# Kernel optimization log

Measured on AMD Instinct MI355X. Metric: run time of the kernel, lower is better.

Reference implementation:

```python
import jax, jax.numpy as jnp
import numpy as np

N, E, F_IN, H, C = 50000, 800000, 64, 4, 32
NEG_SLOPE = 0.2  # PyG GATConv default negative_slope
LN_EPS = 1e-5


def setup_inputs() -> dict:
    key = jax.random.key(0)
    ks = jax.random.split(key, 8)
    s = 1.0 / np.sqrt(F_IN)
    return {
        "x": jax.random.normal(ks[0], (N, F_IN), jnp.float32),
        "edge_index": jax.random.randint(ks[1], (2, E), 0, N, jnp.int64),
        "W": jax.random.normal(ks[2], (F_IN, H * C), jnp.float32) * s,
        "att_src": jax.random.normal(ks[3], (H, C), jnp.float32) * s,
        "att_dst": jax.random.normal(ks[4], (H, C), jnp.float32) * s,
        "bias": jnp.zeros((H * C,), jnp.float32),
        "res_w": jax.random.normal(ks[5], (F_IN, H * C), jnp.float32) * s,
        "res_b": jnp.zeros((H * C,), jnp.float32),
        "ln_g": jnp.ones((H * C,), jnp.float32),
        "ln_b": jnp.zeros((H * C,), jnp.float32),
    }


def reference(x, edge_index, W, att_src, att_dst, bias, res_w, res_b, ln_g, ln_b):
    n = x.shape[0]
    # GATConv adds self-loops by default
    loop = jnp.arange(n, dtype=edge_index.dtype)
    src = jnp.concatenate([edge_index[0], loop])
    dst = jnp.concatenate([edge_index[1], loop])

    h = (x @ W).reshape(n, H, C)                      # [N,H,C]
    a_src = jnp.einsum('nhc,hc->nh', h, att_src)       # [N,H]
    a_dst = jnp.einsum('nhc,hc->nh', h, att_dst)

    e = a_src[src] + a_dst[dst]                        # [Etot,H]
    e = jnp.where(e >= 0, e, NEG_SLOPE * e)            # leaky_relu

    # segment softmax over destination nodes
    m = jax.ops.segment_max(e, dst, num_segments=n)    # [N,H]
    ex = jnp.exp(e - m[dst])
    denom = jax.ops.segment_sum(ex, dst, num_segments=n)
    alpha = ex / denom[dst]                            # [Etot,H]

    msg = h[src] * alpha[:, :, None]                   # [Etot,H,C]
    out = jax.ops.segment_sum(msg, dst, num_segments=n)  # [N,H,C]
    out = out.reshape(n, H * C) + bias

    # elu; dropout is identity in eval mode
    out = jnp.where(out > 0, out, jnp.expm1(out))
    out = out + (x @ res_w + res_b)                    # residual Linear

    mu = out.mean(-1, keepdims=True)
    var = ((out - mu) ** 2).mean(-1, keepdims=True)
    return ln_g * (out - mu) * jax.lax.rsqrt(var + LN_EPS) + ln_b
```

## Files before the change

### kernel.cpp

```cpp
#include <hip/hip_runtime.h>

#define F_IN 64
#define NH 4
#define HC 128
#define NEG_SLOPE 0.2f
#define LN_EPS 1e-5f
#define BUCKET 128
#define BKT_CAP 2560
#define NSC 128
#define KREG 28
#define KW_BLOCKS 64

typedef __bf16 bf16_8 __attribute__((ext_vector_type(8)));
typedef float  f32_4  __attribute__((ext_vector_type(4)));

__device__ inline int detect_is64(const int* __restrict__ ei, int E) {
    int lane = threadIdx.x & 63;
    long long stride = (2LL * E) / 65;
    int w = ei[(((long long)(lane + 1)) * stride) | 1];
    return __ballot(w != 0) == 0ULL;
}

__device__ inline unsigned bfpack(float a, float b) {
    unsigned ua = __float_as_uint(a), ub = __float_as_uint(b);
    ua = (ua + 0x7fffu + ((ua >> 16) & 1u)) >> 16;
    ub = (ub + 0x7fffu + ((ub >> 16) & 1u)) >> 16;
    return ua | (ub << 16);
}

__global__ __launch_bounds__(256) void k_prep(
    const float* __restrict__ W, const float* __restrict__ res_w,
    __bf16* __restrict__ wt, int* __restrict__ g_cnt)
{
    int idx = blockIdx.x * 256 + threadIdx.x;
    int ch = idx >> 6, k = idx & 63;
    const float* src = (ch < HC) ? W : res_w;
    wt[ch * 64 + k] = (__bf16)src[k * HC + (ch & (HC - 1))];
    if (idx < 512) g_cnt[idx] = 0;
}

__global__ __launch_bounds__(256) void k_main(
    const float* __restrict__ x, const __bf16* __restrict__ wt,
    const float* __restrict__ att_src, const float* __restrict__ att_dst,
    unsigned* __restrict__ h_bf, unsigned* __restrict__ r_bf,
    float* __restrict__ a_s, float* __restrict__ a_d, int n,
    const int* __restrict__ ei, int E,
    int* __restrict__ g_cnt, unsigned* __restrict__ epk, int chunk)
{
    __shared__ int bcur[512];
    __shared__ int adj[512];
    __shared__ int ss[256];

    if ((int)blockIdx.x >= NSC) {
        int tid = threadIdx.x;
        int wv_ = tid >> 6, lane = tid & 63;
        int col = lane & 15, quad = lane >> 4;
        int node = (blockIdx.x - NSC) * 64 + wv_ * 16 + col;
        int nrow = (node < n) ? node : (n - 1);

        bf16_8 bx0, bx1;
        {
            const float* xp = &x[nrow * F_IN + quad * 8];
            float4 p0 = *(const float4*)(xp);
            float4 p1 = *(const float4*)(xp + 4);
            float4 p2 = *(const float4*)(xp + 32);
            float4 p3 = *(const float4*)(xp + 36);
            bx0[0] = (__bf16)p0.x; bx0[1] = (__bf16)p0.y; bx0[2] = (__bf16)p0.z; bx0[3] = (__bf16)p0.w;
            bx0[4] = (__bf16)p1.x; bx0[5] = (__bf16)p1.y; bx0[6] = (__bf16)p1.z; bx0[7] = (__bf16)p1.w;
            bx1[0] = (__bf16)p2.x; bx1[1] = (__bf16)p2.y; bx1[2] = (__bf16)p2.z; bx1[3] = (__bf16)p2.w;
            bx1[4] = (__bf16)p3.x; bx1[5] = (__bf16)p3.y; bx1[6] = (__bf16)p3.z; bx1[7] = (__bf16)p3.w;
        }

        float vs[4] = {0.f, 0.f, 0.f, 0.f};
        float vd[4] = {0.f, 0.f, 0.f, 0.f};

#pragma unroll
        for (int mt = 0; mt < 16; ++mt) {
            const __bf16* ap = &wt[(mt * 16 + col) * 64 + quad * 8];
            bf16_8 a0 = *(const bf16_8*)ap;
            bf16_8 a1 = *(const bf16_8*)(ap + 32);
            f32_4 acc = {0.f, 0.f, 0.f, 0.f};
            acc = __builtin_amdgcn_mfma_f32_16x16x32_bf16(a0, bx0, acc, 0, 0, 0);
            acc = __builtin_amdgcn_mfma_f32_16x16x32_bf16(a1, bx1, acc, 0, 0, 0);
            int ch0 = mt * 16 + quad * 4;
            if (mt < 8) {
                float4 as4 = *(const float4*)&att_src[ch0];
                float4 ad4 = *(const float4*)&att_dst[ch0];
                int head = mt >> 1;
                vs[head] += acc[0] * as4.x + acc[1] * as4.y + acc[2] * as4.z + acc[3] * as4.w;
                vd[head] += acc[0] * ad4.x + acc[1] * ad4.y + acc[2] * ad4.z + acc[3] * ad4.w;
                if (node < n) {
                    uint2 pk = make_uint2(bfpack(acc[0], acc[1]), bfpack(acc[2], acc[3]));
                    *(uint2*)&h_bf[node * 64 + (ch0 >> 1)] = pk;
                }
            } else {
                if (node < n) {
                    uint2 pk = make_uint2(bfpack(acc[0], acc[1]), bfpack(acc[2], acc[3]));
                    *(uint2*)&r_bf[node * 64 + ((ch0 - 128) >> 1)] = pk;
                }
            }
        }

#pragma unroll
        for (int hh = 0; hh < NH; ++hh) {
            vs[hh] += __shfl_down(vs[hh], 32, 64);
            vs[hh] += __shfl_down(vs[hh], 16, 64);
            vd[hh] += __shfl_down(vd[hh], 32, 64);
            vd[hh] += __shfl_down(vd[hh], 16, 64);
        }
        if (quad == 0 && node < n) {
            *(float4*)&a_s[node * NH] = make_float4(vs[0], vs[1], vs[2], vs[3]);
            *(float4*)&a_d[node * NH] = make_float4(vd[0], vd[1], vd[2], vd[3]);
        }
        return;
    }

    int t = threadIdx.x;
    for (int i = t; i < 512; i += 256) bcur[i] = 0;
    __syncthreads();
    int is64 = detect_is64(ei, E);
    int base = blockIdx.x * chunk, end = min(E, base + chunk);

    unsigned rg[KREG];
#pragma unroll
    for (int i = 0; i < KREG; ++i) {
        int idx = base + i * 256 + t;
        unsigned ent = 0;
        if (idx < end) {
            int s = is64 ? ei[2 * idx] : ei[idx];
            int d = is64 ? ei[2 * (E + idx)] : ei[E + idx];
            ent = ((unsigned)d << 16) | (unsigned)s;
            atomicAdd(&bcur[d >> 7], 1);
        }
        rg[i] = ent;
    }
    __syncthreads();

    int b0 = 2 * t, b1 = 2 * t + 1;
    int f0 = bcur[b0], f1 = bcur[b1];
    ss[t] = f0 + f1;
    __syncthreads();
#pragma unroll
    for (int off = 1; off < 256; off <<= 1) {
        int u = (t >= off) ? ss[t - off] : 0;
        __syncthreads();
        ss[t] += u;
        __syncthreads();
    }
    int ebase = ss[t] - (f0 + f1);

    int g0 = (f0 > 0) ? atomicAdd(&g_cnt[b0], f0) : 0;
    int g1 = (f1 > 0) ? atomicAdd(&g_cnt[b1], f1) : 0;
    bcur[b0] = ebase;
    bcur[b1] = ebase + f0;
    adj[b0] = b0 * BKT_CAP + g0 - ebase;
    adj[b1] = b1 * BKT_CAP + g1 - (ebase + f0);
    __syncthreads();

#pragma unroll
    for (int i = 0; i < KREG; ++i) {
        int idx = base + i * 256 + t;
        if (idx < end) {
            unsigned ent = rg[i];
            int bb = ent >> 23;
            int p = atomicAdd(&bcur[bb], 1);
            int loc = adj[bb] + p;
            if (loc < (bb + 1) * BKT_CAP) epk[loc] = ent;
        }
    }
}

__global__ __launch_bounds__(256) void kd_sort(
    const int* __restrict__ g_cnt, const unsigned* __restrict__ epk,
    unsigned short* __restrict__ ssorted, unsigned* __restrict__ offdeg, int n)
{
    __shared__ int hist[BUCKET];
    __shared__ int sc[BUCKET];
    __shared__ int cur[BUCKET];
    int b = blockIdx.x, t = threadIdx.x;
    int m = g_cnt[b]; if (m > BKT_CAP) m = BKT_CAP;
    const unsigned* reg = epk + (size_t)b * BKT_CAP;
    if (t < BUCKET) hist[t] = 0;
    __syncthreads();
    for (int e = t; e < m; e += 256)
        atomicAdd(&hist[(reg[e] >> 16) & (BUCKET - 1)], 1);
    __syncthreads();
    if (t < BUCKET) sc[t] = hist[t];
    __syncthreads();
#pragma unroll
    for (int o = 1; o < BUCKET; o <<= 1) {
        int u = (t >= o && t < BUCKET) ? sc[t - o] : 0;
        __syncthreads();
        if (t < BUCKET) sc[t] += u;
        __syncthreads();
    }
    if (t < BUCKET) {
        int excl = sc[t] - hist[t];
        cur[t] = excl;
        int d = b * BUCKET + t;
        if (d < n)
            offdeg[d] = ((unsigned)(b * BKT_CAP + excl) << 12) | (unsigned)hist[t];
    }
    __syncthreads();
    unsigned short* outp = ssorted + (size_t)b * BKT_CAP;
    for (int e = t; e < m; e += 256) {
        unsigned ent = reg[e];
        int p = atomicAdd(&cur[(ent >> 16) & (BUCKET - 1)], 1);
        outp[p] = (unsigned short)(ent & 0xffffu);
    }
}

__global__ __launch_bounds__(256) void k_agg(
    const unsigned* __restrict__ offdeg, const unsigned short* __restrict__ ssorted,
    const float* __restrict__ a_s, const float* __restrict__ a_d,
    const unsigned int* __restrict__ h_bf, const unsigned int* __restrict__ r_bf,
    const float* __restrict__ bias, const float* __restrict__ res_b,
    const float* __restrict__ ln_g, const float* __restrict__ ln_b,
    float* __restrict__ out, int n)
{
    int wv = threadIdx.x >> 6, lane = threadIdx.x & 63;
    int d = blockIdx.x * 4 + wv;
    if (d >= n) return;
    int eh = lane >> 5, g = lane & 31;
    int head = g >> 3;
    float ad = a_d[d * NH + head];

    float a0 = 0.f, a1 = 0.f, a2 = 0.f, a3 = 0.f, denom = 0.f;

    {
        float e = a_s[d * NH + head] + ad;
        e = (e >= 0.f) ? e : NEG_SLOPE * e;
        float w = (eh == 0) ? __expf(e) : 0.f;
        uint2 hv = *(const uint2*)&h_bf[d * 64 + 2 * g];
        a0 += w * __uint_as_float(hv.x << 16);
        a1 += w * __uint_as_float(hv.x & 0xffff0000u);
        a2 += w * __uint_as_float(hv.y << 16);
        a3 += w * __uint_as_float(hv.y & 0xffff0000u);
        denom += w;
    }

    unsigned od = offdeg[d];
    int deg = od & 4095;
    const unsigned short* sl = &ssorted[od >> 12];
    int k = 0;
    for (; k + 7 < deg; k += 8) {
        int s[4]; float ee[4]; uint2 v[4];
#pragma unroll
        for (int i = 0; i < 4; ++i) s[i] = sl[k + 2 * i + eh];
#pragma unroll
        for (int i = 0; i < 4; ++i) ee[i] = a_s[s[i] * NH + head];
#pragma unroll
        for (int i = 0; i < 4; ++i) v[i] = *(const uint2*)&h_bf[s[i] * 64 + 2 * g];
#pragma unroll
        for (int i = 0; i < 4; ++i) {
            float e0 = ee[i] + ad;
            e0 = (e0 >= 0.f) ? e0 : NEG_SLOPE * e0;
            float w0 = __expf(e0);
            denom += w0;
            a0 += w0 * __uint_as_float(v[i].x << 16);
            a1 += w0 * __uint_as_float(v[i].x & 0xffff0000u);
            a2 += w0 * __uint_as_float(v[i].y << 16);
            a3 += w0 * __uint_as_float(v[i].y & 0xffff0000u);
        }
    }
    for (; k < deg; k += 2) {
        int idx = k + eh;
        int valid = idx < deg;
        int s0 = valid ? sl[idx] : 0;
        float e0 = a_s[s0 * NH + head] + ad;
        uint2 v0 = *(const uint2*)&h_bf[s0 * 64 + 2 * g];
        e0 = (e0 >= 0.f) ? e0 : NEG_SLOPE * e0;
        float w0 = valid ? __expf(e0) : 0.f;
        denom += w0;
        a0 += w0 * __uint_as_float(v0.x << 16);
        a1 += w0 * __uint_as_float(v0.x & 0xffff0000u);
        a2 += w0 * __uint_as_float(v0.y << 16);
        a3 += w0 * __uint_as_float(v0.y & 0xffff0000u);
    }

    a0 += __shfl_xor(a0, 32, 64);
    a1 += __shfl_xor(a1, 32, 64);
    a2 += __shfl_xor(a2, 32, 64);
    a3 += __shfl_xor(a3, 32, 64);
    denom += __shfl_xor(denom, 32, 64);

    int c0 = g * 4;
    float4 bi = *(const float4*)&bias[c0];
    float4 rb = *(const float4*)&res_b[c0];
    float4 gg = *(const float4*)&ln_g[c0];
    float4 lb = *(const float4*)&ln_b[c0];
    uint2 rv = *(const uint2*)&r_bf[d * 64 + 2 * g];

    float inv = 1.f / denom;
    float o0 = a0 * inv + bi.x;
    float o1 = a1 * inv + bi.y;
    float o2 = a2 * inv + bi.z;
    float o3 = a3 * inv + bi.w;
    o0 = (o0 > 0.f) ? o0 : expm1f(o0);
    o1 = (o1 > 0.f) ? o1 : expm1f(o1);
    o2 = (o2 > 0.f) ? o2 : expm1f(o2);
    o3 = (o3 > 0.f) ? o3 : expm1f(o3);
    o0 += __uint_as_float(rv.x << 16) + rb.x;
    o1 += __uint_as_float(rv.x & 0xffff0000u) + rb.y;
    o2 += __uint_as_float(rv.y << 16) + rb.z;
    o3 += __uint_as_float(rv.y & 0xffff0000u) + rb.w;

    float ps = o0 + o1 + o2 + o3;
#pragma unroll
    for (int off = 32; off > 0; off >>= 1) ps += __shfl_down(ps, off, 64);
    float mean = __shfl(ps, 0, 64) * (1.f / (2 * HC));
    float d0 = o0 - mean, d1 = o1 - mean, d2 = o2 - mean, d3 = o3 - mean;
    float pv = d0 * d0 + d1 * d1 + d2 * d2 + d3 * d3;
#pragma unroll
    for (int off = 32; off > 0; off >>= 1) pv += __shfl_down(pv, off, 64);
    float var = __shfl(pv, 0, 64) * (1.f / (2 * HC));
    float rs = rsqrtf(var + LN_EPS);
    if (eh == 0) {
        *(float4*)&out[d * HC + c0] =
            make_float4(gg.x * d0 * rs + lb.x, gg.y * d1 * rs + lb.y,
                        gg.z * d2 * rs + lb.z, gg.w * d3 * rs + lb.w);
    }
}

extern "C" void kernel_launch(void* const* d_in, const int* in_sizes, int n_in,
                              void* d_out, int out_size, void* d_ws, size_t ws_size,
                              hipStream_t stream) {
    const float* x       = (const float*)d_in[0];
    const int*   ei      = (const int*)d_in[1];
    const float* W       = (const float*)d_in[2];
    const float* att_src = (const float*)d_in[3];
    const float* att_dst = (const float*)d_in[4];
    const float* bias    = (const float*)d_in[5];
    const float* res_w   = (const float*)d_in[6];
    const float* res_b   = (const float*)d_in[7];
    const float* ln_g    = (const float*)d_in[8];
    const float* ln_b    = (const float*)d_in[9];
    float* out = (float*)d_out;

    int n = in_sizes[0] / F_IN;
    int E = in_sizes[1] / 2;
    int NB = (n + BUCKET - 1) / BUCKET;
    int chunk = (E + NSC - 1) / NSC;
    int nka = (n + 63) / 64;

    unsigned*       h_bf   = (unsigned*)d_ws;
    unsigned*       r_bf   = h_bf + (size_t)n * 64;
    float*          a_s    = (float*)(r_bf + (size_t)n * 64);
    float*          a_d    = a_s + (size_t)n * NH;
    int*            g_cnt  = (int*)(a_d + (size_t)n * NH);
    unsigned*       epk    = (unsigned*)(g_cnt + 512);
    unsigned short* ssd    = (unsigned short*)(epk + (size_t)NB * BKT_CAP);
    unsigned*       offdeg = (unsigned*)(ssd + (size_t)NB * BKT_CAP);
    __bf16*         wt     = (__bf16*)(offdeg + n);

    k_prep<<<KW_BLOCKS, 256, 0, stream>>>(W, res_w, wt, g_cnt);

    k_main<<<NSC + nka, 256, 0, stream>>>(
        x, wt, att_src, att_dst, h_bf, r_bf, a_s, a_d, n,
        ei, E, g_cnt, epk, chunk);

    kd_sort<<<NB, 256, 0, stream>>>(g_cnt, epk, ssd, offdeg, n);

    k_agg<<<(n + 3) / 4, 256, 0, stream>>>(offdeg, ssd, a_s, a_d, h_bf, r_bf,
                                           bias, res_b, ln_g, ln_b, out, n);
}
```

Measured before the change: 169.2 us.

## Process four edges per wave with 16-lane groups and uint4 feature loads

The aggregation kernel now splits each wave into four 16-lane groups, each handling one edge with 8 channels per lane via 128-bit loads, instead of two 32-lane groups with 64-bit loads. The sort kernel pads each destination's segment to an even length so each group can read two source indices with one 32-bit load. The goal is more edges in flight per wave and fewer, wider gather instructions. In exchange it uses more accumulator registers, needs an extra shuffle reduction stage, and swaps expm1f for __expf-1, which loses some accuracy for small negative values.

```diff
diff --git a/kernel.cpp b/kernel.cpp
--- a/kernel.cpp
+++ b/kernel.cpp
@@ -185,7 +185,7 @@
     for (int e = t; e < m; e += 256)
         atomicAdd(&hist[(reg[e] >> 16) & (BUCKET - 1)], 1);
     __syncthreads();
-    if (t < BUCKET) sc[t] = hist[t];
+    if (t < BUCKET) sc[t] = (hist[t] + 1) & ~1;
     __syncthreads();
 #pragma unroll
     for (int o = 1; o < BUCKET; o <<= 1) {
@@ -195,7 +195,7 @@
         __syncthreads();
     }
     if (t < BUCKET) {
-        int excl = sc[t] - hist[t];
+        int excl = sc[t] - ((hist[t] + 1) & ~1);
         cur[t] = excl;
         int d = b * BUCKET + t;
         if (d < n)
@@ -221,21 +221,32 @@
     int wv = threadIdx.x >> 6, lane = threadIdx.x & 63;
     int d = blockIdx.x * 4 + wv;
     if (d >= n) return;
-    int eh = lane >> 5, g = lane & 31;
-    int head = g >> 3;
+    int eh = lane >> 4;
+    int g  = lane & 15;
+    int head = g >> 2;
     float ad = a_d[d * NH + head];
 
-    float a0 = 0.f, a1 = 0.f, a2 = 0.f, a3 = 0.f, denom = 0.f;
+    float ac[8] = {0.f, 0.f, 0.f, 0.f, 0.f, 0.f, 0.f, 0.f};
+    float denom = 0.f;
+
+#define ACCUM(WW, VV)                                                      \
+    do {                                                                   \
+        ac[0] += (WW) * __uint_as_float((VV).x << 16);                     \
+        ac[1] += (WW) * __uint_as_float((VV).x & 0xffff0000u);             \
+        ac[2] += (WW) * __uint_as_float((VV).y << 16);                     \
+        ac[3] += (WW) * __uint_as_float((VV).y & 0xffff0000u);             \
+        ac[4] += (WW) * __uint_as_float((VV).z << 16);                     \
+        ac[5] += (WW) * __uint_as_float((VV).z & 0xffff0000u);             \
+        ac[6] += (WW) * __uint_as_float((VV).w << 16);                     \
+        ac[7] += (WW) * __uint_as_float((VV).w & 0xffff0000u);             \
+    } while (0)
 
     {
         float e = a_s[d * NH + head] + ad;
-        e = (e >= 0.f) ? e : NEG_SLOPE * e;
+        e = fmaxf(e, NEG_SLOPE * e);
         float w = (eh == 0) ? __expf(e) : 0.f;
-        uint2 hv = *(const uint2*)&h_bf[d * 64 + 2 * g];
-        a0 += w * __uint_as_float(hv.x << 16);
-        a1 += w * __uint_as_float(hv.x & 0xffff0000u);
-        a2 += w * __uint_as_float(hv.y << 16);
-        a3 += w * __uint_as_float(hv.y & 0xffff0000u);
+        uint4 hv = *(const uint4*)&h_bf[d * 64 + 4 * g];
+        ACCUM(w, hv);
         denom += w;
     }
 
@@ -244,81 +255,88 @@
     const unsigned short* sl = &ssorted[od >> 12];
     int k = 0;
     for (; k + 7 < deg; k += 8) {
-        int s[4]; float ee[4]; uint2 v[4];
-#pragma unroll
-        for (int i = 0; i < 4; ++i) s[i] = sl[k + 2 * i + eh];
-#pragma unroll
-        for (int i = 0; i < 4; ++i) ee[i] = a_s[s[i] * NH + head];
-#pragma unroll
-        for (int i = 0; i < 4; ++i) v[i] = *(const uint2*)&h_bf[s[i] * 64 + 2 * g];
-#pragma unroll
-        for (int i = 0; i < 4; ++i) {
-            float e0 = ee[i] + ad;
-            e0 = (e0 >= 0.f) ? e0 : NEG_SLOPE * e0;
-            float w0 = __expf(e0);
-            denom += w0;
-            a0 += w0 * __uint_as_float(v[i].x << 16);
-            a1 += w0 * __uint_as_float(v[i].x & 0xffff0000u);
-            a2 += w0 * __uint_as_float(v[i].y << 16);
-            a3 += w0 * __uint_as_float(v[i].y & 0xffff0000u);
-        }
-    }
-    for (; k < deg; k += 2) {
+        unsigned sp = *(const unsigned*)&sl[k + 2 * eh];
+        int s0 = sp & 0xffffu, s1 = sp >> 16;
+        float e0 = a_s[s0 * NH + head];
+        float e1 = a_s[s1 * NH + head];
+        uint4 v0 = *(const uint4*)&h_bf[s0 * 64 + 4 * g];
+        uint4 v1 = *(const uint4*)&h_bf[s1 * 64 + 4 * g];
+        e0 += ad; e0 = fmaxf(e0, NEG_SLOPE * e0);
+        float w0 = __expf(e0);
+        e1 += ad; e1 = fmaxf(e1, NEG_SLOPE * e1);
+        float w1 = __expf(e1);
+        denom += w0 + w1;
+        ACCUM(w0, v0);
+        ACCUM(w1, v1);
+    }
+    for (; k < deg; k += 4) {
         int idx = k + eh;
         int valid = idx < deg;
         int s0 = valid ? sl[idx] : 0;
         float e0 = a_s[s0 * NH + head] + ad;
-        uint2 v0 = *(const uint2*)&h_bf[s0 * 64 + 2 * g];
-        e0 = (e0 >= 0.f) ? e0 : NEG_SLOPE * e0;
+        uint4 v0 = *(const uint4*)&h_bf[s0 * 64 + 4 * g];
+        e0 = fmaxf(e0, NEG_SLOPE * e0);
         float w0 = valid ? __expf(e0) : 0.f;
         denom += w0;
-        a0 += w0 * __uint_as_float(v0.x << 16);
-        a1 += w0 * __uint_as_float(v0.x & 0xffff0000u);
-        a2 += w0 * __uint_as_float(v0.y << 16);
-        a3 += w0 * __uint_as_float(v0.y & 0xffff0000u);
-    }
-
-    a0 += __shfl_xor(a0, 32, 64);
-    a1 += __shfl_xor(a1, 32, 64);
-    a2 += __shfl_xor(a2, 32, 64);
-    a3 += __shfl_xor(a3, 32, 64);
+        ACCUM(w0, v0);
+    }
+#undef ACCUM
+
+#pragma unroll
+    for (int j = 0; j < 8; ++j) {
+        ac[j] += __shfl_xor(ac[j], 32, 64);
+        ac[j] += __shfl_xor(ac[j], 16, 64);
+    }
     denom += __shfl_xor(denom, 32, 64);
-
-    int c0 = g * 4;
-    float4 bi = *(const float4*)&bias[c0];
-    float4 rb = *(const float4*)&res_b[c0];
-    float4 gg = *(const float4*)&ln_g[c0];
-    float4 lb = *(const float4*)&ln_b[c0];
-    uint2 rv = *(const uint2*)&r_bf[d * 64 + 2 * g];
+    denom += __shfl_xor(denom, 16, 64);
+
+    int c0 = g * 8;
+    float4 bi0 = *(const float4*)&bias[c0];
+    float4 bi1 = *(const float4*)&bias[c0 + 4];
+    float4 rb0 = *(const float4*)&res_b[c0];
+    float4 rb1 = *(const float4*)&res_b[c0 + 4];
+    uint4 rv = *(const uint4*)&r_bf[d * 64 + 4 * g];
 
     float inv = 1.f / denom;
-    float o0 = a0 * inv + bi.x;
-    float o1 = a1 * inv + bi.y;
-    float o2 = a2 * inv + bi.z;
-    float o3 = a3 * inv + bi.w;
-    o0 = (o0 > 0.f) ? o0 : expm1f(o0);
-    o1 = (o1 > 0.f) ? o1 : expm1f(o1);
-    o2 = (o2 > 0.f) ? o2 : expm1f(o2);
-    o3 = (o3 > 0.f) ? o3 : expm1f(o3);
-    o0 += __uint_as_float(rv.x << 16) + rb.x;
-    o1 += __uint_as_float(rv.x & 0xffff0000u) + rb.y;
-    o2 += __uint_as_float(rv.y << 16) + rb.z;
-    o3 += __uint_as_float(rv.y & 0xffff0000u) + rb.w;
-
-    float ps = o0 + o1 + o2 + o3;
+    float o[8];
+    o[0] = ac[0] * inv + bi0.x; o[1] = ac[1] * inv + bi0.y;
+    o[2] = ac[2] * inv + bi0.z; o[3] = ac[3] * inv + bi0.w;
+    o[4] = ac[4] * inv + bi1.x; o[5] = ac[5] * inv + bi1.y;
+    o[6] = ac[6] * inv + bi1.z; o[7] = ac[7] * inv + bi1.w;
+#pragma unroll
+    for (int j = 0; j < 8; ++j)
+        o[j] = (o[j] > 0.f) ? o[j] : (__expf(o[j]) - 1.f);
+    o[0] += __uint_as_float(rv.x << 16) + rb0.x;
+    o[1] += __uint_as_float(rv.x & 0xffff0000u) + rb0.y;
+    o[2] += __uint_as_float(rv.y << 16) + rb0.z;
+    o[3] += __uint_as_float(rv.y & 0xffff0000u) + rb0.w;
+    o[4] += __uint_as_float(rv.z << 16) + rb1.x;
+    o[5] += __uint_as_float(rv.z & 0xffff0000u) + rb1.y;
+    o[6] += __uint_as_float(rv.w << 16) + rb1.z;
+    o[7] += __uint_as_float(rv.w & 0xffff0000u) + rb1.w;
+
+    float ps = o[0] + o[1] + o[2] + o[3] + o[4] + o[5] + o[6] + o[7];
 #pragma unroll
     for (int off = 32; off > 0; off >>= 1) ps += __shfl_down(ps, off, 64);
-    float mean = __shfl(ps, 0, 64) * (1.f / (2 * HC));
-    float d0 = o0 - mean, d1 = o1 - mean, d2 = o2 - mean, d3 = o3 - mean;
-    float pv = d0 * d0 + d1 * d1 + d2 * d2 + d3 * d3;
+    float mean = __shfl(ps, 0, 64) * (1.f / (4 * HC));
+    float dv[8], pv = 0.f;
+#pragma unroll
+    for (int j = 0; j < 8; ++j) { dv[j] = o[j] - mean; pv += dv[j] * dv[j]; }
 #pragma unroll
     for (int off = 32; off > 0; off >>= 1) pv += __shfl_down(pv, off, 64);
-    float var = __shfl(pv, 0, 64) * (1.f / (2 * HC));
+    float var = __shfl(pv, 0, 64) * (1.f / (4 * HC));
     float rs = rsqrtf(var + LN_EPS);
     if (eh == 0) {
+        float4 gg0 = *(const float4*)&ln_g[c0];
+        float4 gg1 = *(const float4*)&ln_g[c0 + 4];
+        float4 lb0 = *(const float4*)&ln_b[c0];
+        float4 lb1 = *(const float4*)&ln_b[c0 + 4];
         *(float4*)&out[d * HC + c0] =
-            make_float4(gg.x * d0 * rs + lb.x, gg.y * d1 * rs + lb.y,
-                        gg.z * d2 * rs + lb.z, gg.w * d3 * rs + lb.w);
+            make_float4(gg0.x * dv[0] * rs + lb0.x, gg0.y * dv[1] * rs + lb0.y,
+                        gg0.z * dv[2] * rs + lb0.z, gg0.w * dv[3] * rs + lb0.w);
+        *(float4*)&out[d * HC + c0 + 4] =
+            make_float4(gg1.x * dv[4] * rs + lb1.x, gg1.y * dv[5] * rs + lb1.y,
+                        gg1.z * dv[6] * rs + lb1.z, gg1.w * dv[7] * rs + lb1.w);
     }
 }
 
```

New measurement: 163.7 us. -3.3%, faster.
